# Performance work log

Hardware: AMD Instinct MI355X
Metric: run time of the kernel (lower is better)

## Reference

```python
import jax, jax.numpy as jnp
import numpy as np

DIM = 4096
N_HEADS_Q = 32
N_HEADS_KV = 8
N_REP = N_HEADS_Q // N_HEADS_KV
HEAD_DIM = DIM // N_HEADS_Q


def setup_inputs() -> dict:
    key = jax.random.key(0)
    k0, k1, k2, k3, k4 = jax.random.split(key, 5)
    B, S = 2, 2048
    scale = 1.0 / np.sqrt(DIM)
    return {
        "x": jax.random.normal(k0, (B, S, DIM), dtype=jnp.float32),
        "wq": jax.random.normal(k1, (DIM, N_HEADS_Q * HEAD_DIM), dtype=jnp.float32) * scale,
        "wk": jax.random.normal(k2, (DIM, N_HEADS_KV * HEAD_DIM), dtype=jnp.float32) * scale,
        "wv": jax.random.normal(k3, (DIM, N_HEADS_KV * HEAD_DIM), dtype=jnp.float32) * scale,
        "wo": jax.random.normal(k4, (DIM, DIM), dtype=jnp.float32) * scale,
        "start_pos": 0,
    }


def reference(x, wq, wk, wv, wo, start_pos):
    # use_cache=False path: fresh causal self-attention with GQA.
    B, S, _ = x.shape
    q = (x @ wq).reshape(B, S, N_HEADS_Q, HEAD_DIM)
    k = (x @ wk).reshape(B, S, N_HEADS_KV, HEAD_DIM)
    v = (x @ wv).reshape(B, S, N_HEADS_KV, HEAD_DIM)
    # repeat_kv: each kv head repeated N_REP times contiguously along head axis
    k = jnp.repeat(k, N_REP, axis=2)  # [B, S, Hq, D]
    v = jnp.repeat(v, N_REP, axis=2)
    att = jnp.einsum("bqhd,bkhd->bhqk", q, k) / np.sqrt(HEAD_DIM).astype(np.float32)
    causal = jnp.tril(jnp.ones((S, S), dtype=bool))  # [S, S]
    att = jnp.where(causal[None, None, :, :], att, -jnp.inf)
    scores = jax.nn.softmax(att, axis=-1)
    out = jnp.einsum("bhqk,bkhd->bqhd", scores, v).reshape(B, S, DIM)
    return out @ wo
```

## Files before the change

kernel.cpp:

```cpp
#include <hip/hip_runtime.h>
#include <cstdint>


typedef __bf16 bf16;
typedef __bf16 bf16x4 __attribute__((ext_vector_type(4)));
typedef __bf16 bf16x8 __attribute__((ext_vector_type(8)));
typedef float f32x4 __attribute__((ext_vector_type(4)));
typedef float f32x16 __attribute__((ext_vector_type(16)));

#define DEV_INLINE __device__ __forceinline__

DEV_INLINE void load_lds16(const bf16* g, bf16* l) {
  __builtin_amdgcn_global_load_lds(
      (const __attribute__((address_space(1))) void*)g,
      (__attribute__((address_space(3))) void*)l, 16, 0, 0);
}

DEV_INLINE unsigned pk2(float a, float b) {
  union { bf16 v[2]; unsigned u; } t;
  t.v[0] = (bf16)a; t.v[1] = (bf16)b;
  return t.u;
}

__global__ __launch_bounds__(256) void cast_f32_bf16(const float* __restrict__ in,
                                                     bf16* __restrict__ out, int n) {
  int i = (blockIdx.x * 256 + threadIdx.x) * 8;
  if (i >= n) return;
  float4 a = *(const float4*)(in + i);
  float4 b = *(const float4*)(in + i + 4);
  bf16x8 o;
  o[0] = (bf16)a.x; o[1] = (bf16)a.y; o[2] = (bf16)a.z; o[3] = (bf16)a.w;
  o[4] = (bf16)b.x; o[5] = (bf16)b.y; o[6] = (bf16)b.z; o[7] = (bf16)b.w;
  *(bf16x8*)(out + i) = o;
}

__global__ __launch_bounds__(256) void transpose_cast_all(
    const float* __restrict__ wq, const float* __restrict__ wk,
    const float* __restrict__ wv, const float* __restrict__ wo,
    bf16* __restrict__ wt, bf16* __restrict__ wot, float qscale) {
  __shared__ float t[32][33];
  int bx = blockIdx.x, k0 = blockIdx.y * 32;
  const float* src;
  bf16* dst;
  int N, ncol0, nrow0;
  float scale = 1.0f;
  if (bx < 128) {
    src = wq; dst = wt; N = 4096; ncol0 = bx * 32; nrow0 = ncol0; scale = qscale;
  } else if (bx < 160) {
    src = wk; dst = wt; N = 1024; ncol0 = (bx - 128) * 32; nrow0 = 4096 + ncol0;
  } else if (bx < 192) {
    src = wv; dst = wt; N = 1024; ncol0 = (bx - 160) * 32; nrow0 = 5120 + ncol0;
  } else {
    src = wo; dst = wot; N = 4096; ncol0 = (bx - 192) * 32; nrow0 = ncol0;
  }
  int tx = threadIdx.x, ty = threadIdx.y;
#pragma unroll
  for (int i = 0; i < 32; i += 8)
    t[ty + i][tx] = src[(size_t)(k0 + ty + i) * N + ncol0 + tx];
  __syncthreads();
#pragma unroll
  for (int i = 0; i < 32; i += 8)
    dst[(size_t)(nrow0 + ty + i) * 4096 + k0 + tx] = (bf16)(t[tx][ty + i] * scale);
}

__global__ __launch_bounds__(256) void transpose_v(const bf16* __restrict__ qkv,
                                                   bf16* __restrict__ vt) {
  __shared__ bf16 t[32][33];
  int s0 = blockIdx.x * 32, d0 = blockIdx.y * 32, bh = blockIdx.z;
  int b = bh >> 3, h = bh & 7;
  int tx = threadIdx.x, ty = threadIdx.y;
#pragma unroll
  for (int i = 0; i < 32; i += 8)
    t[ty + i][tx] =
        qkv[(size_t)(b * 2048 + s0 + ty + i) * 6144 + 5120 + h * 128 + d0 + tx];
  __syncthreads();
#pragma unroll
  for (int i = 0; i < 32; i += 8)
    vt[((size_t)bh * 128 + d0 + ty + i) * 2048 + s0 + tx] = t[tx][ty + i];
}

template <typename OT>
__global__ __launch_bounds__(512, 2) void gemm_bt8(const bf16* __restrict__ A,
                                                   const bf16* __restrict__ Bt,
                                                   OT* __restrict__ C,
                                                   int M, int N, int K) {
  __shared__ __align__(16) bf16 lds[2][4][128 * 64];
  const int t = threadIdx.x, w = t >> 6, l = t & 63;
  const int lr = l & 15, lh = l >> 4;
  const int rm = w >> 2, cn = w & 3;
  const int mBase = blockIdx.y * 256, nBase = blockIdx.x * 256;
  const int NT = K >> 6;

  size_t gA0[2], gB0[2];
#pragma unroll
  for (int it = 0; it < 2; it++) {
    int c = it * 512 + t;
    int idx = c >> 3;
    int kc = (c & 7) ^ (idx & 7);
    gA0[it] = (size_t)(mBase + (idx >> 6) * 128 + (idx & 63)) * K + kc * 8;
    gB0[it] = (size_t)(nBase + (idx >> 5) * 64 + (idx & 31)) * K + kc * 8;
  }
  const size_t strideA1 = (size_t)64 * K;
  const size_t strideB1 = (size_t)32 * K;
  const int ldst0 = (w * 64) * 8, ldst1 = (512 + w * 64) * 8;

#define STAGE_Q(tile, q, base, off0, off1)                                  \
  do {                                                                      \
    int th_ = (tile);                                                       \
    if (th_ < NT) {                                                         \
      bf16* qb_ = &lds[th_ & 1][q][0];                                      \
      size_t ka_ = (size_t)th_ * 64;                                        \
      load_lds16((base) + (off0) + ka_, qb_ + ldst0);                       \
      load_lds16((base) + (off1) + ka_, qb_ + ldst1);                       \
    }                                                                       \
  } while (0)
#define STAGE_A0(tile) STAGE_Q(tile, 0, A, gA0[0], gA0[1])
#define STAGE_B0(tile) STAGE_Q(tile, 1, Bt, gB0[0], gB0[1])
#define STAGE_B1(tile) STAGE_Q(tile, 2, Bt, gB0[0] + strideB1, gB0[1] + strideB1)
#define STAGE_A1(tile) STAGE_Q(tile, 3, A, gA0[0] + strideA1, gA0[1] + strideA1)

  STAGE_A0(0); STAGE_B0(0); STAGE_B1(0); STAGE_A1(0);
  STAGE_A0(1); STAGE_B0(1); STAGE_B1(1);

  f32x4 acc[8][4] = {};
  bf16x8 aF[4][2], bF[4][2];
  const int rowA = (rm * 64 + lr) * 64;
  const int colB = (cn * 32 + lr) * 64;
  const int xo0 = ((lh ^ (lr & 7)) << 3);
  const int xo1 = (((4 + lh) ^ (lr & 7)) << 3);

  for (int T = 0; T < NT; T++) {
    if (T < NT - 1) asm volatile("s_waitcnt vmcnt(6)" ::: "memory");
    else            asm volatile("s_waitcnt vmcnt(0)" ::: "memory");
    __builtin_amdgcn_s_barrier();
    const bf16* q0 = &lds[T & 1][0][0];
    const bf16* q1 = &lds[T & 1][1][0];
    const bf16* q2 = &lds[T & 1][2][0];
    const bf16* q3 = &lds[T & 1][3][0];

#pragma unroll
    for (int mi = 0; mi < 4; mi++) {
      aF[mi][0] = *(const bf16x8*)(q0 + rowA + mi * 1024 + xo0);
      aF[mi][1] = *(const bf16x8*)(q0 + rowA + mi * 1024 + xo1);
    }
#pragma unroll
    for (int ni = 0; ni < 2; ni++) {
      bF[ni][0] = *(const bf16x8*)(q1 + colB + ni * 1024 + xo0);
      bF[ni][1] = *(const bf16x8*)(q1 + colB + ni * 1024 + xo1);
    }
    STAGE_A1(T + 1);
    asm volatile("s_waitcnt lgkmcnt(8)" ::: "memory");
    __builtin_amdgcn_s_barrier();
    asm volatile("s_waitcnt lgkmcnt(0)" ::: "memory");
    __builtin_amdgcn_sched_barrier(0);
    __builtin_amdgcn_s_setprio(1);
#pragma unroll
    for (int mi = 0; mi < 4; mi++)
#pragma unroll
      for (int ni = 0; ni < 2; ni++) {
        acc[mi][ni] = __builtin_amdgcn_mfma_f32_16x16x32_bf16(aF[mi][0], bF[ni][0], acc[mi][ni], 0, 0, 0);
        acc[mi][ni] = __builtin_amdgcn_mfma_f32_16x16x32_bf16(aF[mi][1], bF[ni][1], acc[mi][ni], 0, 0, 0);
      }
    __builtin_amdgcn_s_setprio(0);
    __builtin_amdgcn_s_barrier();

#pragma unroll
    for (int ni = 0; ni < 2; ni++) {
      bF[2 + ni][0] = *(const bf16x8*)(q2 + colB + ni * 1024 + xo0);
      bF[2 + ni][1] = *(const bf16x8*)(q2 + colB + ni * 1024 + xo1);
    }
    STAGE_A0(T + 2);
    __builtin_amdgcn_s_barrier();
    asm volatile("s_waitcnt lgkmcnt(0)" ::: "memory");
    __builtin_amdgcn_sched_barrier(0);
    __builtin_amdgcn_s_setprio(1);
#pragma unroll
    for (int mi = 0; mi < 4; mi++)
#pragma unroll
      for (int ni = 2; ni < 4; ni++) {
        acc[mi][ni] = __builtin_amdgcn_mfma_f32_16x16x32_bf16(aF[mi][0], bF[ni][0], acc[mi][ni], 0, 0, 0);
        acc[mi][ni] = __builtin_amdgcn_mfma_f32_16x16x32_bf16(aF[mi][1], bF[ni][1], acc[mi][ni], 0, 0, 0);
      }
    __builtin_amdgcn_s_setprio(0);
    __builtin_amdgcn_s_barrier();

#pragma unroll
    for (int mi = 0; mi < 4; mi++) {
      aF[mi][0] = *(const bf16x8*)(q3 + rowA + mi * 1024 + xo0);
      aF[mi][1] = *(const bf16x8*)(q3 + rowA + mi * 1024 + xo1);
    }
    STAGE_B0(T + 2);
    __builtin_amdgcn_s_barrier();
    asm volatile("s_waitcnt lgkmcnt(0)" ::: "memory");
    __builtin_amdgcn_sched_barrier(0);
    __builtin_amdgcn_s_setprio(1);
#pragma unroll
    for (int mi = 0; mi < 4; mi++)
#pragma unroll
      for (int ni = 0; ni < 2; ni++) {
        acc[4 + mi][ni] = __builtin_amdgcn_mfma_f32_16x16x32_bf16(aF[mi][0], bF[ni][0], acc[4 + mi][ni], 0, 0, 0);
        acc[4 + mi][ni] = __builtin_amdgcn_mfma_f32_16x16x32_bf16(aF[mi][1], bF[ni][1], acc[4 + mi][ni], 0, 0, 0);
      }
    __builtin_amdgcn_s_setprio(0);
    __builtin_amdgcn_s_barrier();

    STAGE_B1(T + 2);
    __builtin_amdgcn_s_barrier();
    __builtin_amdgcn_s_setprio(1);
#pragma unroll
    for (int mi = 0; mi < 4; mi++)
#pragma unroll
      for (int ni = 2; ni < 4; ni++) {
        acc[4 + mi][ni] = __builtin_amdgcn_mfma_f32_16x16x32_bf16(aF[mi][0], bF[ni][0], acc[4 + mi][ni], 0, 0, 0);
        acc[4 + mi][ni] = __builtin_amdgcn_mfma_f32_16x16x32_bf16(aF[mi][1], bF[ni][1], acc[4 + mi][ni], 0, 0, 0);
      }
    __builtin_amdgcn_s_setprio(0);
    __builtin_amdgcn_s_barrier();
  }
#undef STAGE_Q
#undef STAGE_A0
#undef STAGE_B0
#undef STAGE_B1
#undef STAGE_A1

#pragma unroll
  for (int mi = 0; mi < 8; mi++)
#pragma unroll
    for (int ni = 0; ni < 4; ni++) {
      int row = mBase + rm * 128 + mi * 16 + lh * 4;
      int col = nBase + cn * 64 + ni * 16 + lr;
#pragma unroll
      for (int r = 0; r < 4; r++)
        C[(size_t)(row + r) * N + col] = (OT)acc[mi][ni][r];
    }
}

__global__ __launch_bounds__(256, 2) void flash_attn(const bf16* __restrict__ qkv,
                                                     const bf16* __restrict__ vt,
                                                     bf16* __restrict__ ao) {
  __shared__ __align__(16) bf16 Ks[2][64 * 128];
  __shared__ __align__(16) bf16 Vts[2][128 * 64];
  const int t = threadIdx.x, w = t >> 6, l = t & 63;
  const int l31 = l & 31, hi = l >> 5;
  const int h = blockIdx.y, b = blockIdx.z;
  const int hkv = h >> 2;

#define STAGE_KV(kt_, buf_)                                                   \
  do {                                                                        \
    const int kb_ = (kt_) * 64;                                               \
    _Pragma("unroll")                                                         \
    for (int p = 0; p < 4; p++) {                                             \
      int c = p * 256 + t;                                                    \
      int ldsoff = (p * 256 + w * 64) * 8;                                    \
      int krow = c >> 4, kj = (c & 15) ^ (krow & 15);                         \
      load_lds16(qkv + (size_t)(b * 2048 + kb_ + krow) * 6144 + 4096 +        \
                     hkv * 128 + kj * 8,                                      \
                 &Ks[buf_][ldsoff]);                                          \
      int vrow = c >> 3, vj = (c & 7) ^ (vrow & 7);                           \
      load_lds16(vt + ((size_t)(b * 8 + hkv) * 128 + vrow) * 2048 + kb_ +     \
                     vj * 8,                                                  \
                 &Vts[buf_][ldsoff]);                                         \
    }                                                                         \
  } while (0)

  for (int phase = 0; phase < 2; phase++) {
    const int qt = phase == 0 ? blockIdx.x : 15 - blockIdx.x;
    const int qrow0 = qt * 128 + w * 32;
    const int nkt = 2 * qt + 2;
    const int q = qrow0 + l31;

    STAGE_KV(0, 0);

    bf16x8 qf[8];
#pragma unroll
    for (int d0 = 0; d0 < 8; d0++)
      qf[d0] = *(const bf16x8*)&qkv[(size_t)(b * 2048 + q) * 6144 + h * 128 +
                                    d0 * 16 + hi * 8];

    f32x16 oacc[4] = {};
    float mrow = -3.0e38f, lsum = 0.f;

    asm volatile("s_waitcnt vmcnt(0)" ::: "memory");
    __builtin_amdgcn_s_barrier();

    for (int kt = 0; kt < nkt; kt++) {
      const int cur = kt & 1;
      const int kbase = kt * 64;
      if (kt + 1 < nkt) STAGE_KV(kt + 1, cur ^ 1);

      f32x16 s[2] = {};
      __builtin_amdgcn_s_setprio(1);
#pragma unroll
      for (int d0 = 0; d0 < 8; d0++)
#pragma unroll
        for (int ct = 0; ct < 2; ct++) {
          int krow = ct * 32 + l31;
          bf16x8 kf = *(const bf16x8*)&Ks[cur][(krow * 16 +
                                                ((d0 * 2 + hi) ^ (krow & 15))) * 8];
          s[ct] = __builtin_amdgcn_mfma_f32_32x32x16_bf16(kf, qf[d0], s[ct], 0, 0, 0);
        }
      __builtin_amdgcn_s_setprio(0);

      if (kt >= 2 * qt) {
#pragma unroll
        for (int ct = 0; ct < 2; ct++)
#pragma unroll
          for (int reg = 0; reg < 16; reg++) {
            int ki = kbase + ct * 32 + (reg & 3) + 8 * (reg >> 2) + 4 * hi;
            if (ki > q) s[ct][reg] = -3.0e38f;
          }
      }

      float tm[16];
#pragma unroll
      for (int i = 0; i < 16; i++) tm[i] = fmaxf(s[0][i], s[1][i]);
#pragma unroll
      for (int st = 8; st > 0; st >>= 1)
#pragma unroll
        for (int i = 0; i < 8; i++)
          if (i < st) tm[i] = fmaxf(tm[i], tm[i + st]);
      float mx = fmaxf(tm[0], __shfl_xor(tm[0], 32));
      float mnew = fmaxf(mrow, mx);
      float al = exp2f(mrow - mnew);
      mrow = mnew;
#pragma unroll
      for (int ct = 0; ct < 2; ct++)
#pragma unroll
        for (int reg = 0; reg < 16; reg++) s[ct][reg] = exp2f(s[ct][reg] - mnew);
      float ts[16];
#pragma unroll
      for (int i = 0; i < 16; i++) ts[i] = s[0][i] + s[1][i];
#pragma unroll
      for (int st = 8; st > 0; st >>= 1)
#pragma unroll
        for (int i = 0; i < 8; i++)
          if (i < st) ts[i] = ts[i] + ts[i + st];
      float rs = ts[0] + __shfl_xor(ts[0], 32);
      lsum = lsum * al + rs;

#pragma unroll
      for (int db = 0; db < 4; db++)
#pragma unroll
        for (int reg = 0; reg < 16; reg++) oacc[db][reg] *= al;

      bf16x8 pb[4];
#pragma unroll
      for (int ks = 0; ks < 4; ks++) {
        const int ct = ks >> 1, s1 = ks & 1;
        unsigned A0 = pk2(s[ct][(2 * s1) * 4 + 0], s[ct][(2 * s1) * 4 + 1]);
        unsigned A1 = pk2(s[ct][(2 * s1) * 4 + 2], s[ct][(2 * s1) * 4 + 3]);
        unsigned B0 = pk2(s[ct][(2 * s1 + 1) * 4 + 0], s[ct][(2 * s1 + 1) * 4 + 1]);
        unsigned B1 = pk2(s[ct][(2 * s1 + 1) * 4 + 2], s[ct][(2 * s1 + 1) * 4 + 3]);
        unsigned z0 = hi ? A0 : B0, z1 = hi ? A1 : B1;
        unsigned x0 = __shfl_xor(z0, 32), x1 = __shfl_xor(z1, 32);
        union { unsigned u[4]; bf16x8 v; } pw;
        pw.u[0] = hi ? x0 : A0;
        pw.u[1] = hi ? x1 : A1;
        pw.u[2] = hi ? B0 : x0;
        pw.u[3] = hi ? B1 : x1;
        pb[ks] = pw.v;
      }

      __builtin_amdgcn_s_setprio(1);
#pragma unroll
      for (int ks = 0; ks < 4; ks++)
#pragma unroll
        for (int db = 0; db < 4; db++) {
          int vr = db * 32 + l31;
          bf16x8 vf = *(const bf16x8*)&Vts[cur][(vr * 8 +
                                                 ((ks * 2 + hi) ^ (vr & 7))) * 8];
          oacc[db] = __builtin_amdgcn_mfma_f32_32x32x16_bf16(vf, pb[ks], oacc[db], 0, 0, 0);
        }
      __builtin_amdgcn_s_setprio(0);

      asm volatile("s_waitcnt vmcnt(0)" ::: "memory");
      __builtin_amdgcn_s_barrier();
    }

    float inv = 1.0f / lsum;
#pragma unroll
    for (int db = 0; db < 4; db++)
#pragma unroll
      for (int q4 = 0; q4 < 4; q4++) {
        bf16x4 o4;
#pragma unroll
        for (int j = 0; j < 4; j++) o4[j] = (bf16)(oacc[db][q4 * 4 + j] * inv);
        int d0 = db * 32 + q4 * 8 + hi * 4;
        *(bf16x4*)&ao[(size_t)(b * 2048 + q) * 4096 + h * 128 + d0] = o4;
      }
  }
#undef STAGE_KV
}

extern "C" void kernel_launch(void* const* d_in, const int* in_sizes, int n_in,
                              void* d_out, int out_size, void* d_ws, size_t ws_size,
                              hipStream_t stream) {
  const float* x = (const float*)d_in[0];
  const float* wq = (const float*)d_in[1];
  const float* wk = (const float*)d_in[2];
  const float* wv = (const float*)d_in[3];
  const float* wo = (const float*)d_in[4];
  float* out = (float*)d_out;

  char* ws = (char*)d_ws;
  bf16* xb = (bf16*)(ws + 0);
  bf16* wt = (bf16*)(ws + 33554432);
  bf16* wot = (bf16*)(ws + 83886080);
  bf16* qkv = (bf16*)(ws + 117440512);
  bf16* vt = (bf16*)(ws + 167772160);
  bf16* ao = (bf16*)(ws + 176160768);
  if (ws_size < 209715200u) return;

  const float qscale = 0.08838834764831845f * 1.4426950408889634f;

  cast_f32_bf16<<<8192, 256, 0, stream>>>(x, xb, 16777216);
  transpose_cast_all<<<dim3(320, 128), dim3(32, 8), 0, stream>>>(
      wq, wk, wv, wo, wt, wot, qscale);

  gemm_bt8<bf16><<<dim3(24, 16), 512, 0, stream>>>(xb, wt, qkv, 4096, 6144, 4096);
  transpose_v<<<dim3(64, 4, 16), dim3(32, 8), 0, stream>>>(qkv, vt);
  flash_attn<<<dim3(8, 32, 2), 256, 0, stream>>>(qkv, vt, ao);
  gemm_bt8<float><<<dim3(16, 16), 512, 0, stream>>>(ao, wot, out, 4096, 4096, 4096);
}
```

Baseline: 686.6 us.

## Cut barriers in GEMM main loop and split B fragments into lo/hi registers

```diff
diff --git a/kernel.cpp b/kernel.cpp
--- a/kernel.cpp
+++ b/kernel.cpp
@@ -123,7 +123,7 @@
   STAGE_A0(1); STAGE_B0(1); STAGE_B1(1);
 
   f32x4 acc[8][4] = {};
-  bf16x8 aF[4][2], bF[4][2];
+  bf16x8 aF[4][2], bLo[2][2], bHi[2][2];
   const int rowA = (rm * 64 + lr) * 64;
   const int colB = (cn * 32 + lr) * 64;
   const int xo0 = ((lh ^ (lr & 7)) << 3);
@@ -145,77 +145,71 @@
     }
 #pragma unroll
     for (int ni = 0; ni < 2; ni++) {
-      bF[ni][0] = *(const bf16x8*)(q1 + colB + ni * 1024 + xo0);
-      bF[ni][1] = *(const bf16x8*)(q1 + colB + ni * 1024 + xo1);
+      bLo[ni][0] = *(const bf16x8*)(q1 + colB + ni * 1024 + xo0);
+      bLo[ni][1] = *(const bf16x8*)(q1 + colB + ni * 1024 + xo1);
     }
     STAGE_A1(T + 1);
-    asm volatile("s_waitcnt lgkmcnt(8)" ::: "memory");
+
+    __builtin_amdgcn_s_setprio(1);
+#pragma unroll
+    for (int ks = 0; ks < 2; ks++)
+#pragma unroll
+      for (int mi = 0; mi < 4; mi++)
+#pragma unroll
+        for (int ni = 0; ni < 2; ni++)
+          acc[mi][ni] = __builtin_amdgcn_mfma_f32_16x16x32_bf16(
+              aF[mi][ks], bLo[ni][ks], acc[mi][ni], 0, 0, 0);
+    __builtin_amdgcn_s_setprio(0);
+#pragma unroll
+    for (int ni = 0; ni < 2; ni++) {
+      bHi[ni][0] = *(const bf16x8*)(q2 + colB + ni * 1024 + xo0);
+      bHi[ni][1] = *(const bf16x8*)(q2 + colB + ni * 1024 + xo1);
+    }
+
+    __builtin_amdgcn_sched_barrier(0);
     __builtin_amdgcn_s_barrier();
-    asm volatile("s_waitcnt lgkmcnt(0)" ::: "memory");
     __builtin_amdgcn_sched_barrier(0);
+    STAGE_A0(T + 2);
+
     __builtin_amdgcn_s_setprio(1);
 #pragma unroll
-    for (int mi = 0; mi < 4; mi++)
-#pragma unroll
-      for (int ni = 0; ni < 2; ni++) {
-        acc[mi][ni] = __builtin_amdgcn_mfma_f32_16x16x32_bf16(aF[mi][0], bF[ni][0], acc[mi][ni], 0, 0, 0);
-        acc[mi][ni] = __builtin_amdgcn_mfma_f32_16x16x32_bf16(aF[mi][1], bF[ni][1], acc[mi][ni], 0, 0, 0);
-      }
+    for (int ks = 0; ks < 2; ks++)
+#pragma unroll
+      for (int mi = 0; mi < 4; mi++)
+#pragma unroll
+        for (int ni = 0; ni < 2; ni++)
+          acc[mi][2 + ni] = __builtin_amdgcn_mfma_f32_16x16x32_bf16(
+              aF[mi][ks], bHi[ni][ks], acc[mi][2 + ni], 0, 0, 0);
     __builtin_amdgcn_s_setprio(0);
-    __builtin_amdgcn_s_barrier();
-
-#pragma unroll
-    for (int ni = 0; ni < 2; ni++) {
-      bF[2 + ni][0] = *(const bf16x8*)(q2 + colB + ni * 1024 + xo0);
-      bF[2 + ni][1] = *(const bf16x8*)(q2 + colB + ni * 1024 + xo1);
-    }
-    STAGE_A0(T + 2);
-    __builtin_amdgcn_s_barrier();
-    asm volatile("s_waitcnt lgkmcnt(0)" ::: "memory");
-    __builtin_amdgcn_sched_barrier(0);
-    __builtin_amdgcn_s_setprio(1);
-#pragma unroll
-    for (int mi = 0; mi < 4; mi++)
-#pragma unroll
-      for (int ni = 2; ni < 4; ni++) {
-        acc[mi][ni] = __builtin_amdgcn_mfma_f32_16x16x32_bf16(aF[mi][0], bF[ni][0], acc[mi][ni], 0, 0, 0);
-        acc[mi][ni] = __builtin_amdgcn_mfma_f32_16x16x32_bf16(aF[mi][1], bF[ni][1], acc[mi][ni], 0, 0, 0);
-      }
-    __builtin_amdgcn_s_setprio(0);
-    __builtin_amdgcn_s_barrier();
-
 #pragma unroll
     for (int mi = 0; mi < 4; mi++) {
       aF[mi][0] = *(const bf16x8*)(q3 + rowA + mi * 1024 + xo0);
       aF[mi][1] = *(const bf16x8*)(q3 + rowA + mi * 1024 + xo1);
     }
     STAGE_B0(T + 2);
-    __builtin_amdgcn_s_barrier();
-    asm volatile("s_waitcnt lgkmcnt(0)" ::: "memory");
-    __builtin_amdgcn_sched_barrier(0);
+
     __builtin_amdgcn_s_setprio(1);
 #pragma unroll
-    for (int mi = 0; mi < 4; mi++)
-#pragma unroll
-      for (int ni = 0; ni < 2; ni++) {
-        acc[4 + mi][ni] = __builtin_amdgcn_mfma_f32_16x16x32_bf16(aF[mi][0], bF[ni][0], acc[4 + mi][ni], 0, 0, 0);
-        acc[4 + mi][ni] = __builtin_amdgcn_mfma_f32_16x16x32_bf16(aF[mi][1], bF[ni][1], acc[4 + mi][ni], 0, 0, 0);
-      }
+    for (int ks = 0; ks < 2; ks++)
+#pragma unroll
+      for (int mi = 0; mi < 4; mi++)
+#pragma unroll
+        for (int ni = 0; ni < 2; ni++)
+          acc[4 + mi][ni] = __builtin_amdgcn_mfma_f32_16x16x32_bf16(
+              aF[mi][ks], bLo[ni][ks], acc[4 + mi][ni], 0, 0, 0);
     __builtin_amdgcn_s_setprio(0);
-    __builtin_amdgcn_s_barrier();
-
     STAGE_B1(T + 2);
-    __builtin_amdgcn_s_barrier();
+
     __builtin_amdgcn_s_setprio(1);
 #pragma unroll
-    for (int mi = 0; mi < 4; mi++)
-#pragma unroll
-      for (int ni = 2; ni < 4; ni++) {
-        acc[4 + mi][ni] = __builtin_amdgcn_mfma_f32_16x16x32_bf16(aF[mi][0], bF[ni][0], acc[4 + mi][ni], 0, 0, 0);
-        acc[4 + mi][ni] = __builtin_amdgcn_mfma_f32_16x16x32_bf16(aF[mi][1], bF[ni][1], acc[4 + mi][ni], 0, 0, 0);
-      }
+    for (int ks = 0; ks < 2; ks++)
+#pragma unroll
+      for (int mi = 0; mi < 4; mi++)
+#pragma unroll
+        for (int ni = 0; ni < 2; ni++)
+          acc[4 + mi][2 + ni] = __builtin_amdgcn_mfma_f32_16x16x32_bf16(
+              aF[mi][ks], bHi[ni][ks], acc[4 + mi][2 + ni], 0, 0, 0);
     __builtin_amdgcn_s_setprio(0);
-    __builtin_amdgcn_s_barrier();
   }
 #undef STAGE_Q
 #undef STAGE_A0
```

Result: faster. 667.7 us (-2.7%).
